# Kernel tuning notes

Hardware: AMD Instinct MI355X
Metric: run time of the kernel (lower is better)

## Reference

```python
import jax, jax.numpy as jnp
from jax import lax
import numpy as np

IN, H, OUT = 14, 28, 2
B, T = 4096, 512


def setup_inputs() -> dict:
    key = jax.random.key(0)
    ks = jax.random.split(key, 7)
    s_ih = 1.0 / np.sqrt(H)
    return {
        "x": jax.random.normal(ks[0], (B, T, IN), dtype=jnp.float32),
        "W_ih": jax.random.uniform(ks[1], (4 * H, IN), jnp.float32, -s_ih, s_ih),
        "W_hh": jax.random.uniform(ks[2], (4 * H, H), jnp.float32, -s_ih, s_ih),
        "b_ih": jax.random.uniform(ks[3], (4 * H,), jnp.float32, -s_ih, s_ih),
        "b_hh": jax.random.uniform(ks[4], (4 * H,), jnp.float32, -s_ih, s_ih),
        "W_out": jax.random.uniform(ks[5], (OUT, H), jnp.float32, -s_ih, s_ih),
        "b_out": jax.random.uniform(ks[6], (OUT,), jnp.float32, -s_ih, s_ih),
    }


def reference(x, W_ih, W_hh, b_ih, b_hh, W_out, b_out):
    # x: [B, T, IN]; PyTorch LSTM gate order: i, f, g, o
    b, h = x.shape[0], W_hh.shape[1]
    h0 = jnp.zeros((b, h), x.dtype)
    c0 = jnp.zeros((b, h), x.dtype)
    # precompute input projection for all timesteps: [T, B, 4H]
    xg = jnp.einsum('bti,gi->tbg', x, W_ih) + b_ih + b_hh

    def step(carry, xt):
        hp, cp = carry
        gates = xt + hp @ W_hh.T            # [B, 4H]
        i, f, g, o = jnp.split(gates, 4, axis=-1)
        c = jax.nn.sigmoid(f) * cp + jax.nn.sigmoid(i) * jnp.tanh(g)
        hn = jax.nn.sigmoid(o) * jnp.tanh(c)
        return (hn, c), None

    (hT, _), _ = lax.scan(step, (h0, c0), xg)
    # out = Linear(r_out[:, -1, :]) == Linear(h_T)
    return hT @ W_out.T + b_out
```

## Files before the change

kernel.cpp:

```cpp
#include <hip/hip_runtime.h>


#define T_STEPS 512
#define BATCH   4096
#define IN_F    14
#define HID     28
#define OUT_N   2
#define MB      8
#define TC      16
#define NCHUNK  (T_STEPS / TC)
#define HPITCH  40
#define PPITCH  20
#define XREGS   ((MB * TC * IN_F) / 256)

typedef __attribute__((ext_vector_type(8))) short  short8;
typedef __attribute__((ext_vector_type(4))) float  float4v;

#define L1 1.4426950408889634f
#define L2 2.8853900817779268f

__device__ __forceinline__ unsigned short f2bf(float f) {
    union { float f; unsigned int u; } v; v.f = f;
    unsigned int r = (v.u + 0x7FFFu + ((v.u >> 16) & 1u)) >> 16;
    return (unsigned short)r;
}

__global__ __launch_bounds__(256, 2)
void lstm_mfma2(const float* __restrict__ x,
                const float* __restrict__ W_ih,
                const float* __restrict__ W_hh,
                const float* __restrict__ b_ih,
                const float* __restrict__ b_hh,
                const float* __restrict__ W_out,
                const float* __restrict__ b_out,
                float* __restrict__ out) {
    __shared__ __align__(16) short h_a[MB][HPITCH];
    __shared__ __align__(16) short x_a[2][TC][MB][HPITCH];
    __shared__ __align__(16) float pre[4 * HID * PPITCH];
    __shared__ float hfin[MB][HID];

    const int tid = threadIdx.x;
    const int wg  = tid >> 6;
    const int l   = tid & 63;
    const int q   = l >> 4;
    const int m   = l & 15;
    const int mr  = m & 7;
    const int b0  = blockIdx.x * MB;

    short8 bfrag[2][2];
    float  biasf[2];
    #pragma unroll
    for (int nt = 0; nt < 2; ++nt) {
        const int n   = nt * 16 + m;
        const bool vr = (n < HID);
        const int row = wg * HID + (vr ? n : 0);
        biasf[nt] = vr ? (b_ih[row] + b_hh[row]) : 0.0f;
        #pragma unroll
        for (int kt = 0; kt < 2; ++kt) {
            short8 v;
            #pragma unroll
            for (int j = 0; j < 8; ++j) {
                const int k = q * 8 + j;
                float w = 0.0f;
                if (vr) {
                    if (kt == 0) { if (k < HID)  w = W_hh[row * HID + k]; }
                    else         { if (k < IN_F) w = W_ih[row * IN_F + k]; }
                }
                v[j] = (short)f2bf(w);
            }
            bfrag[kt][nt] = v;
        }
    }

    for (int u = tid; u < MB * HPITCH; u += 256) ((short*)h_a)[u] = 0;
    for (int u = tid; u < 2 * TC * MB * HPITCH; u += 256) ((short*)x_a)[u] = 0;

    const float* xbase = x + (long)b0 * T_STEPS * IN_F;
    float xr[XREGS];
    #pragma unroll
    for (int k = 0; k < XREGS; ++k) {
        const int u  = tid + 256 * k;
        const int bb = u / (TC * IN_F);
        const int r  = u - bb * (TC * IN_F);
        xr[k] = xbase[(long)bb * T_STEPS * IN_F + r];
    }
    __syncthreads();

    const int pb = tid & 7;
    const int pu = tid >> 3;
    const bool bact = (pu < HID);
    float c = 0.0f;

    for (int ch = 0; ch < NCHUNK; ++ch) {
        const int buf = ch & 1;
        #pragma unroll
        for (int k = 0; k < XREGS; ++k) {
            const int u  = tid + 256 * k;
            const int bb = u / (TC * IN_F);
            const int r  = u - bb * (TC * IN_F);
            const int t  = r / IN_F;
            const int f  = r - t * IN_F;
            x_a[buf][t][bb][f] = (short)f2bf(xr[k]);
        }
        if (ch + 1 < NCHUNK) {
            #pragma unroll
            for (int k = 0; k < XREGS; ++k) {
                const int u  = tid + 256 * k;
                const int bb = u / (TC * IN_F);
                const int r  = u - bb * (TC * IN_F);
                xr[k] = xbase[(long)bb * T_STEPS * IN_F + (ch + 1) * TC * IN_F + r];
            }
        }
        __syncthreads();

        for (int tt = 0; tt < TC; ++tt) {
            short8 a0 = *(const short8*)&h_a[mr][q * 8];
            short8 a1 = *(const short8*)&x_a[buf][tt][mr][q * 8];
            float4v acc0 = {biasf[0], biasf[0], biasf[0], biasf[0]};
            float4v acc1 = {biasf[1], biasf[1], biasf[1], biasf[1]};
            acc0 = __builtin_amdgcn_mfma_f32_16x16x32_bf16(a0, bfrag[0][0], acc0, 0, 0, 0);
            acc0 = __builtin_amdgcn_mfma_f32_16x16x32_bf16(a1, bfrag[1][0], acc0, 0, 0, 0);
            acc1 = __builtin_amdgcn_mfma_f32_16x16x32_bf16(a0, bfrag[0][1], acc1, 0, 0, 0);
            acc1 = __builtin_amdgcn_mfma_f32_16x16x32_bf16(a1, bfrag[1][1], acc1, 0, 0, 0);
            if (q < 2) {
                *(float4v*)&pre[(wg * HID + m) * PPITCH + q * 4] = acc0;
                if (m < HID - 16)
                    *(float4v*)&pre[(wg * HID + m + 16) * PPITCH + q * 4] = acc1;
            }
            __syncthreads();

            if (bact) {
                float pi = pre[(0 * HID + pu) * PPITCH + pb];
                float pf = pre[(1 * HID + pu) * PPITCH + pb];
                float pg = pre[(2 * HID + pu) * PPITCH + pb];
                float po = pre[(3 * HID + pu) * PPITCH + pb];
                float ei = __builtin_amdgcn_exp2f(pi * (-L1));
                float ef = __builtin_amdgcn_exp2f(pf * (-L1));
                float eg = __builtin_amdgcn_exp2f(pg * (-L2));
                float eo = __builtin_amdgcn_exp2f(po * (-L1));
                float av = 1.0f + ei, bv = 1.0f + ef, dv = 1.0f + eg, vv = 1.0f + eo;
                float pd  = av * dv;
                float pqv = pd * bv;
                float rv  = __builtin_amdgcn_rcpf(pqv);
                float sfv = pd * rv;
                float igv = (1.0f - eg) * bv * rv;
                c = fmaf(sfv, c, igv);
                float ec = __builtin_amdgcn_exp2f(c * (-L2));
                float wv = 1.0f + ec;
                float r2 = __builtin_amdgcn_rcpf(vv * wv);
                float h  = (1.0f - ec) * r2;
                h_a[pb][pu]  = (short)f2bf(h);
                hfin[pb][pu] = h;
            }
            __syncthreads();
        }
    }

    if (tid < MB * OUT_N) {
        const int o  = tid & 1;
        const int bb = tid >> 1;
        float s = b_out[o];
        #pragma unroll
        for (int u = 0; u < HID; ++u)
            s = fmaf(hfin[bb][u], W_out[o * HID + u], s);
        out[(b0 + bb) * OUT_N + o] = s;
    }
}

extern "C" void kernel_launch(void* const* d_in, const int* in_sizes, int n_in,
                              void* d_out, int out_size, void* d_ws, size_t ws_size,
                              hipStream_t stream) {
    const float* x     = (const float*)d_in[0];
    const float* W_ih  = (const float*)d_in[1];
    const float* W_hh  = (const float*)d_in[2];
    const float* b_ih  = (const float*)d_in[3];
    const float* b_hh  = (const float*)d_in[4];
    const float* W_out = (const float*)d_in[5];
    const float* b_out = (const float*)d_in[6];
    float* out = (float*)d_out;

    lstm_mfma2<<<BATCH / MB, 256, 0, stream>>>(
        x, W_ih, W_hh, b_ih, b_hh, W_out, b_out, out);
}
```

Baseline: 335.0 us.

## Fuse gate math into MFMA accumulators and double-buffer hidden state

Transposes the MFMA so weights are the A operand and batch is the N dimension. Each lane's accumulator then holds all four gates (i,f,g,o) for one hidden unit and batch element, and the gate nonlinearity runs directly on MFMA outputs without a shared-memory round trip. Hidden state is double-buffered so each timestep needs one barrier instead of two, and the batch per block doubles to 16 to fill the MFMA N dimension. The trade-off is half as many blocks (256) with launch bounds of one block per SIMD group, which lowers occupancy and latency hiding.

```diff
diff --git a/kernel.cpp b/kernel.cpp
--- a/kernel.cpp
+++ b/kernel.cpp
@@ -6,11 +6,10 @@
 #define IN_F    14
 #define HID     28
 #define OUT_N   2
-#define MB      8
+#define MB      16
 #define TC      16
 #define NCHUNK  (T_STEPS / TC)
 #define HPITCH  40
-#define PPITCH  20
 #define XREGS   ((MB * TC * IN_F) / 256)
 
 typedef __attribute__((ext_vector_type(8))) short  short8;
@@ -25,54 +24,78 @@
     return (unsigned short)r;
 }
 
-__global__ __launch_bounds__(256, 2)
-void lstm_mfma2(const float* __restrict__ x,
-                const float* __restrict__ W_ih,
-                const float* __restrict__ W_hh,
-                const float* __restrict__ b_ih,
-                const float* __restrict__ b_hh,
-                const float* __restrict__ W_out,
-                const float* __restrict__ b_out,
-                float* __restrict__ out) {
-    __shared__ __align__(16) short h_a[MB][HPITCH];
+__device__ __forceinline__ int cvtpk_bf16(float lo, float hi) {
+    int r;
+    asm("v_cvt_pk_bf16_f32 %0, %1, %2" : "=v"(r) : "v"(lo), "v"(hi));
+    return r;
+}
+
+__device__ __forceinline__ void gate4(const float4v pr, float& c, float& hf) {
+    float ei = __builtin_amdgcn_exp2f(pr[0] * (-L1));
+    float ef = __builtin_amdgcn_exp2f(pr[1] * (-L1));
+    float eg = __builtin_amdgcn_exp2f(pr[2] * (-L2));
+    float eo = __builtin_amdgcn_exp2f(pr[3] * (-L1));
+    float av = 1.0f + ei, bv = 1.0f + ef, dv = 1.0f + eg, vv = 1.0f + eo;
+    float pd  = av * dv;
+    float pqv = pd * bv;
+    float rv  = __builtin_amdgcn_rcpf(pqv);
+    float sfv = pd * rv;
+    float igv = (1.0f - eg) * bv * rv;
+    c = fmaf(sfv, c, igv);
+    float ec = __builtin_amdgcn_exp2f(c * (-L2));
+    float wv = 1.0f + ec;
+    float r2 = __builtin_amdgcn_rcpf(vv * wv);
+    hf = (1.0f - ec) * r2;
+}
+
+__global__ __launch_bounds__(256, 1)
+void lstm_fuse(const float* __restrict__ x,
+               const float* __restrict__ W_ih,
+               const float* __restrict__ W_hh,
+               const float* __restrict__ b_ih,
+               const float* __restrict__ b_hh,
+               const float* __restrict__ W_out,
+               const float* __restrict__ b_out,
+               float* __restrict__ out) {
+    __shared__ __align__(16) short h_a[2][MB][HPITCH];
     __shared__ __align__(16) short x_a[2][TC][MB][HPITCH];
-    __shared__ __align__(16) float pre[4 * HID * PPITCH];
     __shared__ float hfin[MB][HID];
 
     const int tid = threadIdx.x;
-    const int wg  = tid >> 6;
+    const int w   = tid >> 6;
     const int l   = tid & 63;
     const int q   = l >> 4;
     const int m   = l & 15;
-    const int mr  = m & 7;
     const int b0  = blockIdx.x * MB;
 
-    short8 bfrag[2][2];
-    float  biasf[2];
+    short8  Ah[2], Ax[2];
+    float4v bias[2];
     #pragma unroll
-    for (int nt = 0; nt < 2; ++nt) {
-        const int n   = nt * 16 + m;
-        const bool vr = (n < HID);
-        const int row = wg * HID + (vr ? n : 0);
-        biasf[nt] = vr ? (b_ih[row] + b_hh[row]) : 0.0f;
+    for (int t = 0; t < 2; ++t) {
+        const int ul = 2 * (m >> 2) + t;
+        const int ug = 8 * w + ul;
+        const bool vr = (ug < HID);
+        const int wrow = (m & 3) * HID + (vr ? ug : 0);
+        short8 vh, vx;
         #pragma unroll
-        for (int kt = 0; kt < 2; ++kt) {
-            short8 v;
-            #pragma unroll
-            for (int j = 0; j < 8; ++j) {
-                const int k = q * 8 + j;
-                float w = 0.0f;
-                if (vr) {
-                    if (kt == 0) { if (k < HID)  w = W_hh[row * HID + k]; }
-                    else         { if (k < IN_F) w = W_ih[row * IN_F + k]; }
-                }
-                v[j] = (short)f2bf(w);
-            }
-            bfrag[kt][nt] = v;
+        for (int j = 0; j < 8; ++j) {
+            const int k = 8 * q + j;
+            float wh = (vr && k < HID)  ? W_hh[wrow * HID + k]  : 0.0f;
+            float wx = (vr && k < IN_F) ? W_ih[wrow * IN_F + k] : 0.0f;
+            vh[j] = (short)f2bf(wh);
+            vx[j] = (short)f2bf(wx);
         }
+        Ah[t] = vh;
+        Ax[t] = vx;
+        const int u = 8 * w + 2 * q + t;
+        float4v bv;
+        #pragma unroll
+        for (int j = 0; j < 4; ++j)
+            bv[j] = (u < HID) ? (b_ih[j * HID + u] + b_hh[j * HID + u]) : 0.0f;
+        bias[t] = bv;
     }
 
-    for (int u = tid; u < MB * HPITCH; u += 256) ((short*)h_a)[u] = 0;
+    for (int u = tid; u < 2 * MB * HPITCH; u += 256) ((short*)h_a)[u] = 0;
     for (int u = tid; u < 2 * TC * MB * HPITCH; u += 256) ((short*)x_a)[u] = 0;
 
     const float* xbase = x + (long)b0 * T_STEPS * IN_F;
@@ -86,10 +109,10 @@
     }
     __syncthreads();
 
-    const int pb = tid & 7;
-    const int pu = tid >> 3;
-    const bool bact = (pu < HID);
-    float c = 0.0f;
+    const int  ug0 = 8 * w + 2 * q;
+    const bool vld = (ug0 < HID);
+    float c0 = 0.0f, c1 = 0.0f, h0f = 0.0f, h1f = 0.0f;
+    int rb = 0;
 
     for (int ch = 0; ch < NCHUNK; ++ch) {
         const int buf = ch & 1;
@@ -114,48 +137,27 @@
         __syncthreads();
 
         for (int tt = 0; tt < TC; ++tt) {
-            short8 a0 = *(const short8*)&h_a[mr][q * 8];
-            short8 a1 = *(const short8*)&x_a[buf][tt][mr][q * 8];
-            float4v acc0 = {biasf[0], biasf[0], biasf[0], biasf[0]};
-            float4v acc1 = {biasf[1], biasf[1], biasf[1], biasf[1]};
-            acc0 = __builtin_amdgcn_mfma_f32_16x16x32_bf16(a0, bfrag[0][0], acc0, 0, 0, 0);
-            acc0 = __builtin_amdgcn_mfma_f32_16x16x32_bf16(a1, bfrag[1][0], acc0, 0, 0, 0);
-            acc1 = __builtin_amdgcn_mfma_f32_16x16x32_bf16(a0, bfrag[0][1], acc1, 0, 0, 0);
-            acc1 = __builtin_amdgcn_mfma_f32_16x16x32_bf16(a1, bfrag[1][1], acc1, 0, 0, 0);
-            if (q < 2) {
-                *(float4v*)&pre[(wg * HID + m) * PPITCH + q * 4] = acc0;
-                if (m < HID - 16)
-                    *(float4v*)&pre[(wg * HID + m + 16) * PPITCH + q * 4] = acc1;
+            short8 bh = *(const short8*)&h_a[rb][m][8 * q];
+            short8 bx = *(const short8*)&x_a[buf][tt][m][8 * q];
+            float4v a0 = __builtin_amdgcn_mfma_f32_16x16x32_bf16(Ax[0], bx, bias[0], 0, 0, 0);
+            float4v a1 = __builtin_amdgcn_mfma_f32_16x16x32_bf16(Ax[1], bx, bias[1], 0, 0, 0);
+            a0 = __builtin_amdgcn_mfma_f32_16x16x32_bf16(Ah[0], bh, a0, 0, 0, 0);
+            a1 = __builtin_amdgcn_mfma_f32_16x16x32_bf16(Ah[1], bh, a1, 0, 0, 0);
+            if (vld) {
+                gate4(a0, c0, h0f);
+                gate4(a1, c1, h1f);
+                *(int*)&h_a[rb ^ 1][m][ug0] = cvtpk_bf16(h0f, h1f);
             }
-            __syncthreads();
-
-            if (bact) {
-                float pi = pre[(0 * HID + pu) * PPITCH + pb];
-                float pf = pre[(1 * HID + pu) * PPITCH + pb];
-                float pg = pre[(2 * HID + pu) * PPITCH + pb];
-                float po = pre[(3 * HID + pu) * PPITCH + pb];
-                float ei = __builtin_amdgcn_exp2f(pi * (-L1));
-                float ef = __builtin_amdgcn_exp2f(pf * (-L1));
-                float eg = __builtin_amdgcn_exp2f(pg * (-L2));
-                float eo = __builtin_amdgcn_exp2f(po * (-L1));
-                float av = 1.0f + ei, bv = 1.0f + ef, dv = 1.0f + eg, vv = 1.0f + eo;
-                float pd  = av * dv;
-                float pqv = pd * bv;
-                float rv  = __builtin_amdgcn_rcpf(pqv);
-                float sfv = pd * rv;
-                float igv = (1.0f - eg) * bv * rv;
-                c = fmaf(sfv, c, igv);
-                float ec = __builtin_amdgcn_exp2f(c * (-L2));
-                float wv = 1.0f + ec;
-                float r2 = __builtin_amdgcn_rcpf(vv * wv);
-                float h  = (1.0f - ec) * r2;
-                h_a[pb][pu]  = (short)f2bf(h);
-                hfin[pb][pu] = h;
-            }
+            rb ^= 1;
             __syncthreads();
         }
     }
 
+    if (vld) {
+        hfin[m][ug0]     = h0f;
+        hfin[m][ug0 + 1] = h1f;
+    }
+    __syncthreads();
     if (tid < MB * OUT_N) {
         const int o  = tid & 1;
         const int bb = tid >> 1;
@@ -179,6 +181,6 @@
     const float* b_out = (const float*)d_in[6];
     float* out = (float*)d_out;
 
-    lstm_mfma2<<<BATCH / MB, 256, 0, stream>>>(
+    lstm_fuse<<<BATCH / MB, 256, 0, stream>>>(
         x, W_ih, W_hh, b_ih, b_hh, W_out, b_out, out);
 }
```

After: 285.4 us. -14.8%, faster.
